# Performance work log

Hardware: AMD Instinct MI355X
Metric: run time of the kernel (lower is better)

Reference implementation:

```python
import jax, jax.numpy as jnp
import numpy as np

C2D, C3D = 256, 128
IA, IB = C2D // 2, C3D // 2  # inter channels: 128, 64
B, H, W = 4, 64, 64


def _conv1x1(x, w, b):
    # x: [B,Cin,H,W], w: [Cout,Cin], b: [Cout]
    return jnp.einsum('oc,bchw->bohw', w, x) + b[None, :, None, None]


def _cross_attn(Q, K, V):
    # Q,K,V: [B,C,H,W] (same C); full HWxHW attention as in the torch code
    Bs, C, h, w = Q.shape
    q = Q.reshape(Bs, C, h * w)
    k = K.reshape(Bs, C, K.shape[2] * K.shape[3])
    v = V.reshape(Bs, C, V.shape[2] * V.shape[3])
    attn = jnp.einsum('bcn,bcm->bnm', q, k) * (C ** -0.5)  # [B,N,M]
    attn = jax.nn.softmax(attn, axis=-1)
    out = jnp.einsum('bnm,bcm->bcn', attn, v)
    return out.reshape(Bs, C, h, w)


def setup_inputs() -> dict:
    key = jax.random.key(0)
    ks = jax.random.split(key, 20)
    def n(k, shape, scale=0.02):
        return jax.random.normal(k, shape, dtype=jnp.float32) * scale
    inp = {
        'features_2d': jax.random.normal(ks[0], (B, C2D, H, W), dtype=jnp.float32),
        'features_3d': jax.random.normal(ks[1], (B, C3D, H, W), dtype=jnp.float32),
        # stream A: Q from 2d, K/V from 3d, all mapped to IA channels
        'wqA': n(ks[2], (IA, C2D)), 'bqA': jnp.zeros((IA,), jnp.float32),
        'wkA': n(ks[3], (IA, C3D)), 'bkA': jnp.zeros((IA,), jnp.float32),
        'wvA': n(ks[4], (IA, C3D)), 'bvA': jnp.zeros((IA,), jnp.float32),
        'wpA': n(ks[5], (C2D, IA)), 'bpA': jnp.zeros((C2D,), jnp.float32),
        # stream B: Q from 3d, K/V from 2d, all mapped to IB channels
        'wqB': n(ks[6], (IB, C3D)), 'bqB': jnp.zeros((IB,), jnp.float32),
        'wkB': n(ks[7], (IB, C2D)), 'bkB': jnp.zeros((IB,), jnp.float32),
        'wvB': n(ks[8], (IB, C2D)), 'bvB': jnp.zeros((IB,), jnp.float32),
        'wpB': n(ks[9], (C3D, IB)), 'bpB': jnp.zeros((C3D,), jnp.float32),
    }
    return inp


def reference(features_2d, features_3d,
              wqA, bqA, wkA, bkA, wvA, bvA, wpA, bpA,
              wqB, bqB, wkB, bkB, wvB, bvB, wpB, bpB):
    Q_A = _conv1x1(features_2d, wqA, bqA)
    K_A = _conv1x1(features_3d, wkA, bkA)
    V_A = _conv1x1(features_3d, wvA, bvA)
    x_2D = features_2d + _conv1x1(_cross_attn(Q_A, K_A, V_A), wpA, bpA)

    Q_B = _conv1x1(features_3d, wqB, bqB)
    K_B = _conv1x1(features_2d, wkB, bkB)
    V_B = _conv1x1(features_2d, wvB, bvB)
    x_3D = features_3d + _conv1x1(_cross_attn(Q_B, K_B, V_B), wpB, bpB)
    return (x_2D, x_3D)
```

## Files before the change

### kernel.cpp

```cpp
#include <hip/hip_runtime.h>
#include <hip/hip_bf16.h>
#include <math.h>

typedef __bf16 bf16_t;
typedef __bf16 bf16x8 __attribute__((ext_vector_type(8)));
typedef float f32x4 __attribute__((ext_vector_type(4)));
typedef float f32x16 __attribute__((ext_vector_type(16)));
typedef unsigned u32x2 __attribute__((ext_vector_type(2)));

#define NPOS 4096
#define LOG2E 1.4426950408889634f

__device__ __forceinline__ f32x4 mfma16(bf16x8 a, bf16x8 b, f32x4 c) {
    return __builtin_amdgcn_mfma_f32_16x16x32_bf16(a, b, c, 0, 0, 0);
}
__device__ __forceinline__ f32x16 mfma32(bf16x8 a, bf16x8 b, f32x16 c) {
    return __builtin_amdgcn_mfma_f32_32x32x16_bf16(a, b, c, 0, 0, 0);
}

typedef __attribute__((address_space(1))) const unsigned gas_u32;
typedef __attribute__((address_space(3))) unsigned las_u32;
__device__ __forceinline__ void gl_lds16(const char* g, char* l) {
    __builtin_amdgcn_global_load_lds((gas_u32*)g, (las_u32*)l, 16, 0, 0);
}

__device__ __forceinline__ float fexp2(float x) {
    float r; asm("v_exp_f32 %0, %1" : "=v"(r) : "v"(x)); return r;
}

#define BARC(N) do {                                                          \
    asm volatile("s_waitcnt vmcnt(" #N ") lgkmcnt(0)" ::: "memory");          \
    __builtin_amdgcn_sched_barrier(0);                                        \
    __builtin_amdgcn_s_barrier();                                             \
    __builtin_amdgcn_sched_barrier(0);                                        \
} while (0)

__device__ __forceinline__ char* sel3(char* a, char* b, char* c, int i) {
    return i == 0 ? a : (i == 1 ? b : c);
}

template<int BYTES>
__device__ __forceinline__ void stG(char* lds, const char* g, int w, int lane) {
    constexpr int NC = BYTES / 4096;
#pragma unroll
    for (int c = 0; c < NC; ++c) {
        int j = (w * NC + c) * 1024 + lane * 16;
        gl_lds16(g + (j ^ (((j >> 8) & 15) << 4)), lds + j);
    }
}
template<int BYTES>
__device__ __forceinline__ void stV(char* lds, const char* g, int w, int lane) {
    constexpr int NC = BYTES / 4096;
#pragma unroll
    for (int c = 0; c < NC; ++c) {
        int j = (w * NC + c) * 1024 + lane * 16;
        int row = j >> 8;
        int col = (j & 255) ^ ((row & 15) << 4);
        int d = (row << 1) | (col >> 7);
        gl_lds16(g + (size_t)d * (NPOS * 2) + (col & 127), lds + j);
    }
}
template<int BYTES>
__device__ __forceinline__ void stV32(char* lds, const char* g, int w, int lane) {
    constexpr int NC = BYTES / 4096;
#pragma unroll
    for (int c = 0; c < NC; ++c) {
        int j = (w * NC + c) * 1024 + lane * 16;
        int row = j >> 8;
        int col = (j & 255) ^ ((row & 15) << 4);
        int d = (row << 2) | (col >> 6);
        gl_lds16(g + (size_t)d * (NPOS * 2) + (col & 63), lds + j);
    }
}

template<int D>
__device__ __forceinline__ bf16x8 ldK(const char* lds, int key, int dbyte) {
    if constexpr (D == 128) {
        return *(const bf16x8*)(lds + key * 256 + (dbyte ^ ((key & 15) << 4)));
    } else {
        int row = key >> 1;
        int col = ((key & 1) << 7) | dbyte;
        return *(const bf16x8*)(lds + row * 256 + (col ^ ((row & 15) << 4)));
    }
}
__device__ __forceinline__ bf16x8 ldV(const char* lds, int d, int kbyte) {
    int row = d >> 1;
    int col = ((d & 1) << 7) | kbyte;
    return *(const bf16x8*)(lds + row * 256 + (col ^ ((row & 15) << 4)));
}
__device__ __forceinline__ bf16x8 ldV32(const char* lds, int d, int kbyte) {
    int row = d >> 2;
    int col = ((d & 3) << 6) | kbyte;
    return *(const bf16x8*)(lds + row * 256 + (col ^ ((row & 15) << 4)));
}

__device__ __forceinline__ unsigned pkbf(float a, float b) {
    union { bf16_t h[2]; unsigned u; } t;
    t.h[0] = (bf16_t)a; t.h[1] = (bf16_t)b;
    return t.u;
}
#define MKPA(sb, base) ({                                                   \
    unsigned a0_ = pkbf((sb)[(base)+0], (sb)[(base)+1]);                    \
    unsigned a1_ = pkbf((sb)[(base)+2], (sb)[(base)+3]);                    \
    unsigned a2_ = pkbf((sb)[(base)+4], (sb)[(base)+5]);                    \
    unsigned a3_ = pkbf((sb)[(base)+6], (sb)[(base)+7]);                    \
    u32x2 r0_ = __builtin_amdgcn_permlane32_swap(a2_, a0_, false, false);   \
    u32x2 r1_ = __builtin_amdgcn_permlane32_swap(a3_, a1_, false, false);   \
    union { unsigned u[4]; bf16x8 v; } pu_;                                 \
    pu_.u[0] = r0_.y; pu_.u[1] = r1_.y; pu_.u[2] = r0_.x; pu_.u[3] = r1_.x; \
    pu_.v; })

__global__ __launch_bounds__(256) void k_trw(const float* __restrict__ s2d,
                                             const float* __restrict__ s3d,
                                             bf16_t* __restrict__ d2d,
                                             bf16_t* __restrict__ d3d,
                                             const float* w0, const float* w1, const float* w2, const float* w3,
                                             const float* w4, const float* w5, const float* w6, const float* w7,
                                             bf16_t* wdst)
{
    __shared__ float tile[64][65];
    int bid = blockIdx.x, tid = threadIdx.x;
    if (bid >= 1536) {
        int i = (bid - 1536) * 256 + tid;
        if      (i <  32768) wdst[i] = (bf16_t)w0[i];
        else if (i <  49152) wdst[i] = (bf16_t)w1[i - 32768];
        else if (i <  65536) wdst[i] = (bf16_t)w2[i - 49152];
        else if (i <  98304) wdst[i] = (bf16_t)w3[i - 65536];
        else if (i < 106496) wdst[i] = (bf16_t)w4[i - 98304];
        else if (i < 122880) wdst[i] = (bf16_t)w5[i - 106496];
        else if (i < 139264) wdst[i] = (bf16_t)w6[i - 122880];
        else if (i < 147456) wdst[i] = (bf16_t)w7[i - 139264];
        return;
    }
    const float* src; bf16_t* dst; int C, b, c0, n0;
    if (bid < 1024) { src = s2d; dst = d2d; C = 256; b = bid >> 8; c0 = ((bid >> 6) & 3) << 6; n0 = (bid & 63) << 6; }
    else { int r = bid - 1024; src = s3d; dst = d3d; C = 128; b = r >> 7; c0 = ((r >> 6) & 1) << 6; n0 = (r & 63) << 6; }
    const float* sp = src + ((size_t)b * C + c0) * NPOS + n0;
#pragma unroll
    for (int i = 0; i < 16; i++) {
        int idx = tid + i * 256; int c = idx >> 6, n = idx & 63;
        tile[c][n] = sp[(size_t)c * NPOS + n];
    }
    __syncthreads();
    bf16_t* dp = dst + ((size_t)b * NPOS + n0) * C + c0;
#pragma unroll
    for (int i = 0; i < 16; i++) {
        int idx = tid + i * 256; int n = idx >> 6, c = idx & 63;
        dp[(size_t)n * C + c] = (bf16_t)tile[c][n];
    }
}

template<int K, int MQ, int MK, int MV>
__device__ void prod_body(const bf16_t* __restrict__ Xt,
                          const bf16_t* __restrict__ wq, const float* __restrict__ bq, float sq,
                          const bf16_t* __restrict__ wk, const float* __restrict__ bk,
                          const bf16_t* __restrict__ wv, const float* __restrict__ bv,
                          bf16_t* __restrict__ Qo, bf16_t* __restrict__ Ko, bf16_t* __restrict__ Vo,
                          char* smem, int bid, int tid)
{
    constexpr int RB = K * 2;
    int b = bid >> 6, n0 = (bid & 63) << 6;
    int wave = tid >> 6, lane = tid & 63, g = lane >> 4, lr = lane & 15;

    const char* src = (const char*)(Xt + ((size_t)b * NPOS + n0) * K);
#pragma unroll
    for (int j0 = 0; j0 < 64 * RB; j0 += 4096) {
        int j = j0 + tid * 16;
        int row = j / RB;
        int col = j & (RB - 1);
        float4 v = *(const float4*)(src + (size_t)row * RB + col);
        *(float4*)(smem + row * RB + (col ^ ((row & 7) << 4))) = v;
    }
    __syncthreads();

    f32x4 aq[MQ / 16], ak[MK / 16], av[MV / 16];
#pragma unroll
    for (int ob = 0; ob < MQ / 16; ++ob) aq[ob] = f32x4{0.f,0.f,0.f,0.f};
#pragma unroll
    for (int ob = 0; ob < MK / 16; ++ob) ak[ob] = f32x4{0.f,0.f,0.f,0.f};
#pragma unroll
    for (int ob = 0; ob < MV / 16; ++ob) av[ob] = f32x4{0.f,0.f,0.f,0.f};
    int xrow = wave * 16 + lr;
#pragma unroll
    for (int ks = 0; ks < K / 32; ++ks) {
        bf16x8 xf = *(const bf16x8*)(smem + xrow * RB + ((((ks * 32 + g * 8) * 2)) ^ ((xrow & 7) << 4)));
#pragma unroll
        for (int ob = 0; ob < MQ / 16; ++ob) {
            bf16x8 wf = *(const bf16x8*)(wq + (size_t)(ob * 16 + lr) * K + ks * 32 + g * 8);
            aq[ob] = mfma16(xf, wf, aq[ob]);
        }
#pragma unroll
        for (int ob = 0; ob < MK / 16; ++ob) {
            bf16x8 wf = *(const bf16x8*)(wk + (size_t)(ob * 16 + lr) * K + ks * 32 + g * 8);
            ak[ob] = mfma16(xf, wf, ak[ob]);
        }
#pragma unroll
        for (int ob = 0; ob < MV / 16; ++ob) {
            bf16x8 wf = *(const bf16x8*)(wv + (size_t)(ob * 16 + lr) * K + ks * 32 + g * 8);
            av[ob] = mfma16(wf, xf, av[ob]);
        }
    }
#pragma unroll
    for (int ob = 0; ob < MQ / 16; ++ob) {
        int o = ob * 16 + lr;
        float bs = bq[o];
#pragma unroll
        for (int r = 0; r < 4; r++) {
            size_t n = (size_t)b * NPOS + n0 + wave * 16 + g * 4 + r;
            Qo[n * MQ + o] = (bf16_t)((aq[ob][r] + bs) * sq);
        }
    }
#pragma unroll
    for (int ob = 0; ob < MK / 16; ++ob) {
        int o = ob * 16 + lr;
        float bs = bk[o];
#pragma unroll
        for (int r = 0; r < 4; r++) {
            size_t n = (size_t)b * NPOS + n0 + wave * 16 + g * 4 + r;
            Ko[n * MK + o] = (bf16_t)(ak[ob][r] + bs);
        }
    }
#pragma unroll
    for (int ob = 0; ob < MV / 16; ++ob) {
#pragma unroll
        for (int r = 0; r < 4; r++) {
            int o = ob * 16 + g * 4 + r;
            size_t idx = ((size_t)b * MV + o) * NPOS + n0 + wave * 16 + lr;
            Vo[idx] = (bf16_t)(av[ob][r] + bv[o]);
        }
    }
}

__global__ __launch_bounds__(256, 2) void k_prodm(const bf16_t* ft2d, const bf16_t* ft3d,
                                                  const bf16_t* wbf,
                                                  const float* bqA, const float* bkA, const float* bvA,
                                                  const float* bqB, const float* bkB, const float* bvB,
                                                  bf16_t* QtA, bf16_t* KtA_, bf16_t* VA_,
                                                  bf16_t* QtB, bf16_t* KtB_, bf16_t* VB_)
{
    extern __shared__ char smem[];
    const float sA = 0.08838834764831845f * LOG2E;
    const float sB = 0.125f * LOG2E;
    if (blockIdx.x < 256)
        prod_body<256, 128, 64, 64>(ft2d, wbf + 0, bqA, sA,
                                    wbf + 106496, bkB, wbf + 122880, bvB,
                                    QtA, KtB_, VB_, smem, blockIdx.x, threadIdx.x);
    else
        prod_body<128, 64, 128, 128>(ft3d, wbf + 98304, bqB, sB,
                                     wbf + 32768, bkA, wbf + 49152, bvA,
                                     QtB, KtA_, VA_, smem, blockIdx.x - 256, threadIdx.x);
}

template<int K, int M>
__device__ void out_body(const bf16_t* __restrict__ Xt,
                         const float* __restrict__ lp,
                         const bf16_t* __restrict__ W,
                         const float* __restrict__ bias,
                         const float* __restrict__ resid,
                         float* __restrict__ outp,
                         char* smem, int bid, int tid)
{
    constexpr int RB = K * 2;
    int b = bid >> 6, n0 = (bid & 63) << 6;
    int wave = tid >> 6, lane = tid & 63, g = lane >> 4, lr = lane & 15;

#pragma unroll
    for (int j0 = 0; j0 < 64 * RB; j0 += 4096) {
        int j = j0 + tid * 16;
        int row = j / RB;
        int colb = j & (RB - 1);
        size_t n = (size_t)b * NPOS + n0 + row;
        float l1 = lp[n], l2 = lp[16384 + n];
        float inv = 1.f / (l1 + l2);
        float w1 = l1 * inv, w2 = l2 * inv;
        bf16x8 o1 = *(const bf16x8*)(Xt + n * K + (colb >> 1));
        bf16x8 o2 = *(const bf16x8*)(Xt + (size_t)16384 * K + n * K + (colb >> 1));
        bf16x8 xv;
#pragma unroll
        for (int e = 0; e < 8; ++e) xv[e] = (bf16_t)(w1 * (float)o1[e] + w2 * (float)o2[e]);
        *(bf16x8*)(smem + row * RB + (colb ^ ((row & 7) << 4))) = xv;
    }
    __syncthreads();

    f32x4 acc[M / 16];
#pragma unroll
    for (int ob = 0; ob < M / 16; ++ob) acc[ob] = f32x4{0.f,0.f,0.f,0.f};
    int xrow = wave * 16 + lr;
#pragma unroll
    for (int ks = 0; ks < K / 32; ++ks) {
        bf16x8 xf = *(const bf16x8*)(smem + xrow * RB + ((((ks * 32 + g * 8) * 2)) ^ ((xrow & 7) << 4)));
#pragma unroll
        for (int ob = 0; ob < M / 16; ++ob) {
            bf16x8 wf = *(const bf16x8*)(W + (size_t)(ob * 16 + lr) * K + ks * 32 + g * 8);
            acc[ob] = mfma16(wf, xf, acc[ob]);
        }
    }
#pragma unroll
    for (int ob = 0; ob < M / 16; ++ob) {
#pragma unroll
        for (int r = 0; r < 4; r++) {
            int o = ob * 16 + g * 4 + r;
            size_t idx = ((size_t)b * M + o) * NPOS + n0 + wave * 16 + lr;
            outp[idx] = acc[ob][r] + bias[o] + resid[idx];
        }
    }
}

__global__ __launch_bounds__(256, 2) void k_outm(const bf16_t* OtHA, const float* lHA,
                                                 const bf16_t* OtHB, const float* lHB,
                                                 const bf16_t* wbf,
                                                 const float* bpA, const float* f2d,
                                                 const float* bpB, const float* f3d,
                                                 float* out)
{
    extern __shared__ char smem[];
    if (blockIdx.x < 256)
        out_body<128, 256>(OtHA, lHA, wbf + 65536, bpA, f2d, out, smem, blockIdx.x, threadIdx.x);
    else
        out_body<64, 128>(OtHB, lHB, wbf + 139264, bpB, f3d, out + 4194304, smem, blockIdx.x - 256, threadIdx.x);
}

__device__ void attnA11(const bf16_t* __restrict__ Qt, const bf16_t* __restrict__ Kt,
                        const bf16_t* __restrict__ V, bf16_t* __restrict__ OtH,
                        float* __restrict__ lH, int b, int qblk, int half,
                        char* smem, int tid)
{
    char* Kb0 = smem;          char* Kb1 = smem + 8192;  char* Kb2 = smem + 16384;
    char* Vb0 = smem + 24576;  char* Vb1 = smem + 32768; char* Vb2 = smem + 40960;
    int w = tid >> 6, lane = tid & 63;
    int qcol = lane & 31, hi = lane >> 5;
    int q0 = qblk * 128 + w * 32;

    bf16x8 qf[8];
    const bf16_t* qp = Qt + ((size_t)b * NPOS + q0 + qcol) * 128 + hi * 8;
#pragma unroll
    for (int ks = 0; ks < 8; ++ks) qf[ks] = *(const bf16x8*)(qp + ks * 16);

    f32x16 acc[4];
#pragma unroll
    for (int cb = 0; cb < 4; ++cb)
#pragma unroll
        for (int i = 0; i < 16; ++i) acc[cb][i] = 0.f;
    float l_c = 0.f;

    const char* kg = (const char*)(Kt + (size_t)b * NPOS * 128) + (size_t)half * 64 * 8192;
    const char* vg = (const char*)(V + (size_t)b * 128 * NPOS) + (size_t)half * 4096;

    stG<8192>(Kb0, kg, w, lane);
    stV32<8192>(Vb0, vg, w, lane);
    stG<8192>(Kb1, kg + 8192, w, lane);
    stV32<8192>(Vb1, vg + 64, w, lane);
    BARC(4);

    f32x16 sE, sO;
#pragma unroll
    for (int i = 0; i < 16; ++i) sE[i] = 0.f;
#pragma unroll
    for (int ks = 0; ks < 8; ++ks)
        sE = mfma32(ldK<128>(Kb0, qcol, ks * 32 + hi * 16), qf[ks], sE);
    stG<8192>(Kb2, kg + 16384, w, lane);
    BARC(2);

    int ce = 0;
#pragma unroll 1
    for (int t2 = 0; t2 < 32; ++t2) {
        int t = 2 * t2;
        int c1 = ce + 1; if (c1 > 2) c1 -= 3;
        int c2 = ce + 2; if (c2 > 2) c2 -= 3;
        {
            int tK = t + 3; if (tK > 63) tK = 63;
            int tV = t + 2; if (tV > 63) tV = 63;
            stG<8192>(sel3(Kb0, Kb1, Kb2, ce), kg + (size_t)tK * 8192, w, lane);
            stV32<8192>(sel3(Vb0, Vb1, Vb2, c2), vg + (size_t)tV * 64, w, lane);
            const char* Kn = sel3(Kb0, Kb1, Kb2, c1);
#pragma unroll
            for (int i = 0; i < 16; ++i) sO[i] = 0.f;
            __builtin_amdgcn_s_setprio(1);
#pragma unroll
            for (int ks = 0; ks < 8; ++ks)
                sO = mfma32(ldK<128>(Kn, qcol, ks * 32 + hi * 16), qf[ks], sO);
            __builtin_amdgcn_s_setprio(0);
            float ps = 0.f;
#pragma unroll
            for (int i = 0; i < 16; ++i) { float e = fexp2(sE[i]); sE[i] = e; ps += e; }
            ps += __shfl_xor(ps, 32);
            l_c += ps;
            bf16x8 pa0 = MKPA(sE, 0), pa1 = MKPA(sE, 8);
            const char* Vc = sel3(Vb0, Vb1, Vb2, ce);
            __builtin_amdgcn_s_setprio(1);
#pragma unroll
            for (int cb = 0; cb < 4; ++cb) {
                int d = cb * 32 + qcol;
                acc[cb] = mfma32(pa0, ldV32(Vc, d, hi * 16), acc[cb]);
                acc[cb] = mfma32(pa1, ldV32(Vc, d, 32 + hi * 16), acc[cb]);
            }
            __builtin_amdgcn_s_setprio(0);
            BARC(4);
        }
        {
            int tK = t + 4; if (tK > 63) tK = 63;
            int tV = t + 3; if (tV > 63) tV = 63;
            stG<8192>(sel3(Kb0, Kb1, Kb2, c1), kg + (size_t)tK * 8192, w, lane);
            stV32<8192>(sel3(Vb0, Vb1, Vb2, ce), vg + (size_t)tV * 64, w, lane);
            const char* Kn = sel3(Kb0, Kb1, Kb2, c2);
#pragma unroll
            for (int i = 0; i < 16; ++i) sE[i] = 0.f;
            __builtin_amdgcn_s_setprio(1);
#pragma unroll
            for (int ks = 0; ks < 8; ++ks)
                sE = mfma32(ldK<128>(Kn, qcol, ks * 32 + hi * 16), qf[ks], sE);
            __builtin_amdgcn_s_setprio(0);
            float ps = 0.f;
#pragma unroll
            for (int i = 0; i < 16; ++i) { float e = fexp2(sO[i]); sO[i] = e; ps += e; }
            ps += __shfl_xor(ps, 32);
            l_c += ps;
            bf16x8 pa0 = MKPA(sO, 0), pa1 = MKPA(sO, 8);
            const char* Vc = sel3(Vb0, Vb1, Vb2, c1);
            __builtin_amdgcn_s_setprio(1);
#pragma unroll
            for (int cb = 0; cb < 4; ++cb) {
                int d = cb * 32 + qcol;
                acc[cb] = mfma32(pa0, ldV32(Vc, d, hi * 16), acc[cb]);
                acc[cb] = mfma32(pa1, ldV32(Vc, d, 32 + hi * 16), acc[cb]);
            }
            __builtin_amdgcn_s_setprio(0);
            BARC(4);
        }
        ce = c2;
    }

    float linv = 1.f / l_c;
    size_t obase = (size_t)(half * 4 + b) * NPOS;
#pragma unroll
    for (int r = 0; r < 16; ++r) {
        int crow = (r & 3) + 8 * (r >> 2) + 4 * hi;
        float lr = __shfl(linv, crow);
        size_t nrow = obase + q0 + crow;
#pragma unroll
        for (int cb = 0; cb < 4; ++cb)
            OtH[nrow * 128 + cb * 32 + qcol] = (bf16_t)(acc[cb][r] * lr);
    }
    if (lane < 32) lH[obase + q0 + lane] = l_c;
}

__device__ void attnB11(const bf16_t* __restrict__ Qt, const bf16_t* __restrict__ Kt,
                        const bf16_t* __restrict__ V, bf16_t* __restrict__ OtH,
                        float* __restrict__ lH, int b, int qblk, int half,
                        char* smem, int tid)
{
    char* Kb0 = smem;          char* Kb1 = smem + 8192;  char* Kb2 = smem + 16384;
    char* Vb0 = smem + 24576;  char* Vb1 = smem + 32768; char* Vb2 = smem + 40960;
    int w = tid >> 6, lane = tid & 63;
    int qcol = lane & 31, hi = lane >> 5;
    int q0 = qblk * 128 + w * 32;

    bf16x8 qf[4];
    const bf16_t* qp = Qt + ((size_t)b * NPOS + q0 + qcol) * 64 + hi * 8;
#pragma unroll
    for (int ks = 0; ks < 4; ++ks) qf[ks] = *(const bf16x8*)(qp + ks * 16);

    f32x16 acc[2];
#pragma unroll
    for (int cb = 0; cb < 2; ++cb)
#pragma unroll
        for (int i = 0; i < 16; ++i) acc[cb][i] = 0.f;
    float l_c = 0.f;

    const char* kg = (const char*)(Kt + (size_t)b * NPOS * 64) + (size_t)half * 32 * 8192;
    const char* vg = (const char*)(V + (size_t)b * 64 * NPOS) + (size_t)half * 4096;

    stG<8192>(Kb0, kg, w, lane);
    stV<8192>(Vb0, vg, w, lane);
    stG<8192>(Kb1, kg + 8192, w, lane);
    stV<8192>(Vb1, vg + 128, w, lane);
    BARC(4);

    f32x16 sE0, sE1, sO0, sO1;
#pragma unroll
    for (int i = 0; i < 16; ++i) { sE0[i] = 0.f; sE1[i] = 0.f; }
#pragma unroll
    for (int ks = 0; ks < 4; ++ks) {
        int dbyte = ks * 32 + hi * 16;
        sE0 = mfma32(ldK<64>(Kb0, qcol, dbyte), qf[ks], sE0);
        sE1 = mfma32(ldK<64>(Kb0, 32 + qcol, dbyte), qf[ks], sE1);
    }
    stG<8192>(Kb2, kg + 16384, w, lane);
    BARC(2);

    int ce = 0;
#pragma unroll 1
    for (int t2 = 0; t2 < 16; ++t2) {
        int t = 2 * t2;
        int c1 = ce + 1; if (c1 > 2) c1 -= 3;
        int c2 = ce + 2; if (c2 > 2) c2 -= 3;
        {
            int tK = t + 3; if (tK > 31) tK = 31;
            int tV = t + 2; if (tV > 31) tV = 31;
            stG<8192>(sel3(Kb0, Kb1, Kb2, ce), kg + (size_t)tK * 8192, w, lane);
            stV<8192>(sel3(Vb0, Vb1, Vb2, c2), vg + (size_t)tV * 128, w, lane);
            const char* Kn = sel3(Kb0, Kb1, Kb2, c1);
#pragma unroll
            for (int i = 0; i < 16; ++i) { sO0[i] = 0.f; sO1[i] = 0.f; }
            __builtin_amdgcn_s_setprio(1);
#pragma unroll
            for (int ks = 0; ks < 4; ++ks) {
                int dbyte = ks * 32 + hi * 16;
                sO0 = mfma32(ldK<64>(Kn, qcol, dbyte), qf[ks], sO0);
                sO1 = mfma32(ldK<64>(Kn, 32 + qcol, dbyte), qf[ks], sO1);
            }
            __builtin_amdgcn_s_setprio(0);
            float ps = 0.f;
#pragma unroll
            for (int i = 0; i < 16; ++i) { float e = fexp2(sE0[i]); sE0[i] = e; ps += e; }
#pragma unroll
            for (int i = 0; i < 16; ++i) { float e = fexp2(sE1[i]); sE1[i] = e; ps += e; }
            ps += __shfl_xor(ps, 32);
            l_c += ps;
            bf16x8 pa0 = MKPA(sE0, 0), pa1 = MKPA(sE0, 8);
            bf16x8 pa2 = MKPA(sE1, 0), pa3 = MKPA(sE1, 8);
            const char* Vc = sel3(Vb0, Vb1, Vb2, ce);
            __builtin_amdgcn_s_setprio(1);
#pragma unroll
            for (int cb = 0; cb < 2; ++cb) {
                int d = cb * 32 + qcol;
                acc[cb] = mfma32(pa0, ldV(Vc, d, 0  + hi * 16), acc[cb]);
                acc[cb] = mfma32(pa1, ldV(Vc, d, 32 + hi * 16), acc[cb]);
                acc[cb] = mfma32(pa2, ldV(Vc, d, 64 + hi * 16), acc[cb]);
                acc[cb] = mfma32(pa3, ldV(Vc, d, 96 + hi * 16), acc[cb]);
            }
            __builtin_amdgcn_s_setprio(0);
            BARC(4);
        }
        {
            int tK = t + 4; if (tK > 31) tK = 31;
            int tV = t + 3; if (tV > 31) tV = 31;
            stG<8192>(sel3(Kb0, Kb1, Kb2, c1), kg + (size_t)tK * 8192, w, lane);
            stV<8192>(sel3(Vb0, Vb1, Vb2, ce), vg + (size_t)tV * 128, w, lane);
            const char* Kn = sel3(Kb0, Kb1, Kb2, c2);
#pragma unroll
            for (int i = 0; i < 16; ++i) { sE0[i] = 0.f; sE1[i] = 0.f; }
            __builtin_amdgcn_s_setprio(1);
#pragma unroll
            for (int ks = 0; ks < 4; ++ks) {
                int dbyte = ks * 32 + hi * 16;
                sE0 = mfma32(ldK<64>(Kn, qcol, dbyte), qf[ks], sE0);
                sE1 = mfma32(ldK<64>(Kn, 32 + qcol, dbyte), qf[ks], sE1);
            }
            __builtin_amdgcn_s_setprio(0);
            float ps = 0.f;
#pragma unroll
            for (int i = 0; i < 16; ++i) { float e = fexp2(sO0[i]); sO0[i] = e; ps += e; }
#pragma unroll
            for (int i = 0; i < 16; ++i) { float e = fexp2(sO1[i]); sO1[i] = e; ps += e; }
            ps += __shfl_xor(ps, 32);
            l_c += ps;
            bf16x8 pa0 = MKPA(sO0, 0), pa1 = MKPA(sO0, 8);
            bf16x8 pa2 = MKPA(sO1, 0), pa3 = MKPA(sO1, 8);
            const char* Vc = sel3(Vb0, Vb1, Vb2, c1);
            __builtin_amdgcn_s_setprio(1);
#pragma unroll
            for (int cb = 0; cb < 2; ++cb) {
                int d = cb * 32 + qcol;
                acc[cb] = mfma32(pa0, ldV(Vc, d, 0  + hi * 16), acc[cb]);
                acc[cb] = mfma32(pa1, ldV(Vc, d, 32 + hi * 16), acc[cb]);
                acc[cb] = mfma32(pa2, ldV(Vc, d, 64 + hi * 16), acc[cb]);
                acc[cb] = mfma32(pa3, ldV(Vc, d, 96 + hi * 16), acc[cb]);
            }
            __builtin_amdgcn_s_setprio(0);
            BARC(4);
        }
        ce = c2;
    }

    float linv = 1.f / l_c;
    size_t obase = (size_t)(half * 4 + b) * NPOS;
#pragma unroll
    for (int r = 0; r < 16; ++r) {
        int crow = (r & 3) + 8 * (r >> 2) + 4 * hi;
        float lr = __shfl(linv, crow);
        size_t nrow = obase + q0 + crow;
#pragma unroll
        for (int cb = 0; cb < 2; ++cb)
            OtH[nrow * 64 + cb * 32 + qcol] = (bf16_t)(acc[cb][r] * lr);
    }
    if (lane < 32) lH[obase + q0 + lane] = l_c;
}

__global__ __launch_bounds__(256, 2) void k_attn11(const bf16_t* QtA, const bf16_t* KtA, const bf16_t* VA,
                                                   bf16_t* OtHA, float* lHA,
                                                   const bf16_t* QtB, const bf16_t* KtB, const bf16_t* VB,
                                                   bf16_t* OtHB, float* lHB)
{
    extern __shared__ char smem[];
    int bid = blockIdx.x, tid = threadIdx.x;
    if (bid < 256) {
        int x = bid & 7;
        attnA11(QtA, KtA, VA, OtHA, lHA, x >> 1, bid >> 3, x & 1, smem, tid);
    } else {
        int u = bid - 256;
        int x = u & 7;
        attnB11(QtB, KtB, VB, OtHB, lHB, x >> 1, u >> 3, x & 1, smem, tid);
    }
}

extern "C" void kernel_launch(void* const* d_in, const int* in_sizes, int n_in,
                              void* d_out, int out_size, void* d_ws, size_t ws_size,
                              hipStream_t stream)
{
    (void)in_sizes; (void)n_in; (void)out_size; (void)ws_size;
    const float* f2d = (const float*)d_in[0];
    const float* f3d = (const float*)d_in[1];
    const float* wqA = (const float*)d_in[2];  const float* bqA = (const float*)d_in[3];
    const float* wkA = (const float*)d_in[4];  const float* bkA = (const float*)d_in[5];
    const float* wvA = (const float*)d_in[6];  const float* bvA = (const float*)d_in[7];
    const float* wpA = (const float*)d_in[8];  const float* bpA = (const float*)d_in[9];
    const float* wqB = (const float*)d_in[10]; const float* bqB = (const float*)d_in[11];
    const float* wkB = (const float*)d_in[12]; const float* bkB = (const float*)d_in[13];
    const float* wvB = (const float*)d_in[14]; const float* bvB = (const float*)d_in[15];
    const float* wpB = (const float*)d_in[16]; const float* bpB = (const float*)d_in[17];

    char* ws = (char*)d_ws;
    bf16_t* ft2d = (bf16_t*)(ws);
    bf16_t* ft3d = (bf16_t*)(ws + 8388608);
    bf16_t* wbf  = (bf16_t*)(ws + 12582912);
    bf16_t* QtA  = (bf16_t*)(ws + 12877824);
    bf16_t* KtA_ = (bf16_t*)(ws + 17072128);
    bf16_t* VA_  = (bf16_t*)(ws + 21266432);
    bf16_t* QtB  = (bf16_t*)(ws + 25460736);
    bf16_t* KtB_ = (bf16_t*)(ws + 27557888);
    bf16_t* VB_  = (bf16_t*)(ws + 29655040);
    bf16_t* OtHA = (bf16_t*)(ws);
    float*  lHA  = (float*)(ws + 8388608);
    bf16_t* OtHB = (bf16_t*)(ws + 31752192);
    float*  lHB  = (float*)(ws + 35946496);

    k_trw<<<2112, 256, 0, stream>>>(f2d, f3d, ft2d, ft3d,
                                    wqA, wkA, wvA, wpA, wqB, wkB, wvB, wpB, wbf);

    k_prodm<<<512, 256, 32768, stream>>>(ft2d, ft3d, wbf,
        bqA, bkA, bvA, bqB, bkB, bvB,
        QtA, KtA_, VA_, QtB, KtB_, VB_);

    k_attn11<<<512, 256, 49152, stream>>>(QtA, KtA_, VA_, OtHA, lHA, QtB, KtB_, VB_, OtHB, lHB);

    k_outm<<<512, 256, 16384, stream>>>(OtHA, lHA, OtHB, lHB, wbf,
        bpA, f2d, bpB, f3d, (float*)d_out);
}
```

Baseline: 121.4 us.

## Split stream-A attention KV range four ways and merge partials in output projection

Stream A attention now splits the key/value range into four chunks instead of two, doubling the number of A blocks (768 total blocks). Each split writes normalized partial outputs and row sums to separate buffers, and the output-projection kernel combines the four partials weighted by their sums before the GEMM. Launch bounds are raised to 3 blocks per SM to help occupancy. The aim is to balance work between the heavier A stream and the B stream and fill the GPU better, at the cost of more partial-output traffic and extra merge arithmetic in the output kernel.

Result: slower. 138.3 us (+13.9%).

```diff
diff --git a/kernel.cpp b/kernel.cpp
--- a/kernel.cpp
+++ b/kernel.cpp
@@ -251,6 +251,64 @@
                                      QtB, KtA_, VA_, smem, blockIdx.x - 256, threadIdx.x);
 }
 
+__device__ void out_bodyA4(const bf16_t* __restrict__ Xt,
+                           const bf16_t* __restrict__ Xt3,
+                           const float* __restrict__ lp,
+                           const bf16_t* __restrict__ W,
+                           const float* __restrict__ bias,
+                           const float* __restrict__ resid,
+                           float* __restrict__ outp,
+                           char* smem, int bid, int tid)
+{
+    constexpr int K = 128, M = 256, RB = 256;
+    int b = bid >> 6, n0 = (bid & 63) << 6;
+    int wave = tid >> 6, lane = tid & 63, g = lane >> 4, lr = lane & 15;
+
+#pragma unroll
+    for (int j0 = 0; j0 < 64 * RB; j0 += 4096) {
+        int j = j0 + tid * 16;
+        int row = j >> 8;
+        int colb = j & 255;
+        size_t n = (size_t)b * NPOS + n0 + row;
+        float l0 = lp[n], l1 = lp[16384 + n], l2 = lp[32768 + n], l3 = lp[49152 + n];
+        float inv = 1.f / (l0 + l1 + l2 + l3);
+        bf16x8 o0 = *(const bf16x8*)(Xt  + (size_t)0 * 2097152 + n * K + (colb >> 1));
+        bf16x8 o1 = *(const bf16x8*)(Xt  + (size_t)1 * 2097152 + n * K + (colb >> 1));
+        bf16x8 o2 = *(const bf16x8*)(Xt  + (size_t)2 * 2097152 + n * K + (colb >> 1));
+        bf16x8 o3 = *(const bf16x8*)(Xt3 + n * K + (colb >> 1));
+        float w0 = l0 * inv, w1 = l1 * inv, w2 = l2 * inv, w3 = l3 * inv;
+        bf16x8 xv;
+#pragma unroll
+        for (int e = 0; e < 8; ++e)
+            xv[e] = (bf16_t)(w0 * (float)o0[e] + w1 * (float)o1[e] + w2 * (float)o2[e] + w3 * (float)o3[e]);
+        *(bf16x8*)(smem + row * RB + (colb ^ ((row & 7) << 4))) = xv;
+    }
+    __syncthreads();
+
+    f32x4 acc[M / 16];
+#pragma unroll
+    for (int ob = 0; ob < M / 16; ++ob) acc[ob] = f32x4{0.f,0.f,0.f,0.f};
+    int xrow = wave * 16 + lr;
+#pragma unroll
+    for (int ks = 0; ks < K / 32; ++ks) {
+        bf16x8 xf = *(const bf16x8*)(smem + xrow * RB + ((((ks * 32 + g * 8) * 2)) ^ ((xrow & 7) << 4)));
+#pragma unroll
+        for (int ob = 0; ob < M / 16; ++ob) {
+            bf16x8 wf = *(const bf16x8*)(W + (size_t)(ob * 16 + lr) * K + ks * 32 + g * 8);
+            acc[ob] = mfma16(wf, xf, acc[ob]);
+        }
+    }
+#pragma unroll
+    for (int ob = 0; ob < M / 16; ++ob) {
+#pragma unroll
+        for (int r = 0; r < 4; r++) {
+            int o = ob * 16 + g * 4 + r;
+            size_t idx = ((size_t)b * M + o) * NPOS + n0 + wave * 16 + lr;
+            outp[idx] = acc[ob][r] + bias[o] + resid[idx];
+        }
+    }
+}
+
 template<int K, int M>
 __device__ void out_body(const bf16_t* __restrict__ Xt,
                          const float* __restrict__ lp,
@@ -306,7 +364,7 @@
     }
 }
 
-__global__ __launch_bounds__(256, 2) void k_outm(const bf16_t* OtHA, const float* lHA,
+__global__ __launch_bounds__(256, 2) void k_outm(const bf16_t* OtHA, const bf16_t* OtHA3, const float* lHA,
                                                  const bf16_t* OtHB, const float* lHB,
                                                  const bf16_t* wbf,
                                                  const float* bpA, const float* f2d,
@@ -315,14 +373,14 @@
 {
     extern __shared__ char smem[];
     if (blockIdx.x < 256)
-        out_body<128, 256>(OtHA, lHA, wbf + 65536, bpA, f2d, out, smem, blockIdx.x, threadIdx.x);
+        out_bodyA4(OtHA, OtHA3, lHA, wbf + 65536, bpA, f2d, out, smem, blockIdx.x, threadIdx.x);
     else
         out_body<64, 128>(OtHB, lHB, wbf + 139264, bpB, f3d, out + 4194304, smem, blockIdx.x - 256, threadIdx.x);
 }
 
-__device__ void attnA11(const bf16_t* __restrict__ Qt, const bf16_t* __restrict__ Kt,
-                        const bf16_t* __restrict__ V, bf16_t* __restrict__ OtH,
-                        float* __restrict__ lH, int b, int qblk, int half,
+__device__ void attnA15(const bf16_t* __restrict__ Qt, const bf16_t* __restrict__ Kt,
+                        const bf16_t* __restrict__ V, bf16_t* __restrict__ Op,
+                        float* __restrict__ lH, int b, int qblk, int split,
                         char* smem, int tid)
 {
     char* Kb0 = smem;          char* Kb1 = smem + 8192;  char* Kb2 = smem + 16384;
@@ -343,8 +401,8 @@
         for (int i = 0; i < 16; ++i) acc[cb][i] = 0.f;
     float l_c = 0.f;
 
-    const char* kg = (const char*)(Kt + (size_t)b * NPOS * 128) + (size_t)half * 64 * 8192;
-    const char* vg = (const char*)(V + (size_t)b * 128 * NPOS) + (size_t)half * 4096;
+    const char* kg = (const char*)(Kt + (size_t)b * NPOS * 128) + (size_t)split * 32 * 8192;
+    const char* vg = (const char*)(V + (size_t)b * 128 * NPOS) + (size_t)split * 2048;
 
     stG<8192>(Kb0, kg, w, lane);
     stV32<8192>(Vb0, vg, w, lane);
@@ -363,13 +421,13 @@
 
     int ce = 0;
 #pragma unroll 1
-    for (int t2 = 0; t2 < 32; ++t2) {
+    for (int t2 = 0; t2 < 16; ++t2) {
         int t = 2 * t2;
         int c1 = ce + 1; if (c1 > 2) c1 -= 3;
         int c2 = ce + 2; if (c2 > 2) c2 -= 3;
         {
-            int tK = t + 3; if (tK > 63) tK = 63;
-            int tV = t + 2; if (tV > 63) tV = 63;
+            int tK = t + 3; if (tK > 31) tK = 31;
+            int tV = t + 2; if (tV > 31) tV = 31;
             stG<8192>(sel3(Kb0, Kb1, Kb2, ce), kg + (size_t)tK * 8192, w, lane);
             stV32<8192>(sel3(Vb0, Vb1, Vb2, c2), vg + (size_t)tV * 64, w, lane);
             const char* Kn = sel3(Kb0, Kb1, Kb2, c1);
@@ -398,8 +456,8 @@
             BARC(4);
         }
         {
-            int tK = t + 4; if (tK > 63) tK = 63;
-            int tV = t + 3; if (tV > 63) tV = 63;
+            int tK = t + 4; if (tK > 31) tK = 31;
+            int tV = t + 3; if (tV > 31) tV = 31;
             stG<8192>(sel3(Kb0, Kb1, Kb2, c1), kg + (size_t)tK * 8192, w, lane);
             stV32<8192>(sel3(Vb0, Vb1, Vb2, ce), vg + (size_t)tV * 64, w, lane);
             const char* Kn = sel3(Kb0, Kb1, Kb2, c2);
@@ -431,17 +489,17 @@
     }
 
     float linv = 1.f / l_c;
-    size_t obase = (size_t)(half * 4 + b) * NPOS;
+    size_t obase = (size_t)b * NPOS + q0;
 #pragma unroll
     for (int r = 0; r < 16; ++r) {
         int crow = (r & 3) + 8 * (r >> 2) + 4 * hi;
         float lr = __shfl(linv, crow);
-        size_t nrow = obase + q0 + crow;
+        size_t nrow = obase + crow;
 #pragma unroll
         for (int cb = 0; cb < 4; ++cb)
-            OtH[nrow * 128 + cb * 32 + qcol] = (bf16_t)(acc[cb][r] * lr);
-    }
-    if (lane < 32) lH[obase + q0 + lane] = l_c;
+            Op[nrow * 128 + cb * 32 + qcol] = (bf16_t)(acc[cb][r] * lr);
+    }
+    if (lane < 32) lH[split * 16384 + b * NPOS + q0 + lane] = l_c;
 }
 
 __device__ void attnB11(const bf16_t* __restrict__ Qt, const bf16_t* __restrict__ Kt,
@@ -587,18 +645,20 @@
     if (lane < 32) lH[obase + q0 + lane] = l_c;
 }
 
-__global__ __launch_bounds__(256, 2) void k_attn11(const bf16_t* QtA, const bf16_t* KtA, const bf16_t* VA,
-                                                   bf16_t* OtHA, float* lHA,
+__global__ __launch_bounds__(256, 3) void k_attn15(const bf16_t* QtA, const bf16_t* KtA, const bf16_t* VA,
+                                                   bf16_t* OtHA, bf16_t* OtHA3, float* lHA,
                                                    const bf16_t* QtB, const bf16_t* KtB, const bf16_t* VB,
                                                    bf16_t* OtHB, float* lHB)
 {
     extern __shared__ char smem[];
     int bid = blockIdx.x, tid = threadIdx.x;
-    if (bid < 256) {
-        int x = bid & 7;
-        attnA11(QtA, KtA, VA, OtHA, lHA, x >> 1, bid >> 3, x & 1, smem, tid);
+    if (bid < 512) {
+        int x = bid & 7, u = bid >> 3;
+        int b = x >> 1, split = (x & 1) * 2 + (u & 1), qblk = u >> 1;
+        bf16_t* op = (split < 3) ? OtHA + (size_t)split * 2097152 : OtHA3;
+        attnA15(QtA, KtA, VA, op, lHA, b, qblk, split, smem, tid);
     } else {
-        int u = bid - 256;
+        int u = bid - 512;
         int x = u & 7;
         attnB11(QtB, KtB, VB, OtHB, lHB, x >> 1, u >> 3, x & 1, smem, tid);
     }
@@ -630,10 +690,11 @@
     bf16_t* QtB  = (bf16_t*)(ws + 25460736);
     bf16_t* KtB_ = (bf16_t*)(ws + 27557888);
     bf16_t* VB_  = (bf16_t*)(ws + 29655040);
-    bf16_t* OtHA = (bf16_t*)(ws);
-    float*  lHA  = (float*)(ws + 8388608);
     bf16_t* OtHB = (bf16_t*)(ws + 31752192);
     float*  lHB  = (float*)(ws + 35946496);
+    bf16_t* OtHA  = (bf16_t*)(ws);
+    bf16_t* OtHA3 = (bf16_t*)(ws + 36077568);
+    float*  lHA   = (float*)(ws + 40271872);
 
     k_trw<<<2112, 256, 0, stream>>>(f2d, f3d, ft2d, ft3d,
                                     wqA, wkA, wvA, wpA, wqB, wkB, wvB, wpB, wbf);
@@ -642,8 +703,9 @@
         bqA, bkA, bvA, bqB, bkB, bvB,
         QtA, KtA_, VA_, QtB, KtB_, VB_);
 
-    k_attn11<<<512, 256, 49152, stream>>>(QtA, KtA_, VA_, OtHA, lHA, QtB, KtB_, VB_, OtHB, lHB);
-
-    k_outm<<<512, 256, 16384, stream>>>(OtHA, lHA, OtHB, lHB, wbf,
+    k_attn15<<<768, 256, 49152, stream>>>(QtA, KtA_, VA_, OtHA, OtHA3, lHA,
+                                          QtB, KtB_, VB_, OtHB, lHB);
+
+    k_outm<<<512, 256, 16384, stream>>>(OtHA, OtHA3, lHA, OtHB, lHB, wbf,
         bpA, f2d, bpB, f3d, (float*)d_out);
 }
```
